# Optimization experiments

Measured on AMD Instinct MI355X. Metric: run time of the kernel, lower is better.

The kernel has to match this reference:

```python
import jax, jax.numpy as jnp
import numpy as np

BATCH = 16384
N_IN = 128
CTX = 128
H = 1024
NB = 8                      # num_bins
OUT_MULT = 3 * NB - 1       # widths + heights + derivatives for RQS
TAIL = 3.0                  # tail_bound
SCALE = float(np.sqrt((H * H) // 2))  # sqrt(prod(hidden_dims)//len(hidden_dims))
MIN_W = 1e-3; MIN_H = 1e-3; MIN_D = 1e-3
DPAD = float(np.log(np.exp(1.0 - MIN_D) - 1.0))  # softplus(DPAD)+MIN_D == 1 at boundaries


def _masks():
    # Standard sequential MADE masks. Input degrees 1..n_in, hidden degrees cycle.
    deg_in = np.arange(1, N_IN + 1)
    deg_h = (np.arange(H) % (N_IN - 1)) + 1
    m0 = deg_h[:, None] >= deg_in[None, :]          # [H, N_IN]
    m1 = deg_h[:, None] >= deg_h[None, :]           # [H, H]
    deg_out = np.repeat(deg_in, OUT_MULT)           # matches view(b, n_in, out_mult)
    m2 = deg_out[:, None] > deg_h[None, :]          # [N_IN*OUT_MULT, H]
    return jnp.asarray(m0), jnp.asarray(m1), jnp.asarray(m2)


def setup_inputs() -> dict:
    key = jax.random.key(0)
    k = jax.random.split(key, 6)
    def rn(kk, shape, fan_in):
        return (jax.random.normal(kk, shape, dtype=jnp.float32) * np.sqrt(1.0 / fan_in)).astype(jnp.float32)
    m0, m1, m2 = _masks()
    return {
        "x": jax.random.normal(k[0], (BATCH, N_IN), dtype=jnp.float32),
        "context": jax.random.normal(k[1], (BATCH, CTX), dtype=jnp.float32),
        "ctx_w": rn(k[2], (H, CTX), CTX),
        "w0": rn(k[3], (H, N_IN), N_IN), "b0": jnp.zeros((H,), jnp.float32),
        "w1": rn(k[4], (H, H), H),       "b1": jnp.zeros((H,), jnp.float32),
        "w2": rn(k[5], (N_IN * OUT_MULT, H), H), "b2": jnp.zeros((N_IN * OUT_MULT,), jnp.float32),
        "mask0": m0, "mask1": m1, "mask2": m2,
    }


def _rqs(x, uw, uh, ud):
    # x: [B, D]; uw, uh: [B, D, NB]; ud: [B, D, NB-1]
    inside = jnp.abs(x) <= TAIL
    xc = jnp.clip(x, -TAIL, TAIL)

    w = MIN_W + (1.0 - MIN_W * NB) * jax.nn.softmax(uw, axis=-1)
    cw = jnp.cumsum(w, axis=-1)
    cw = jnp.concatenate([jnp.zeros_like(cw[..., :1]), cw], axis=-1)
    cw = 2.0 * TAIL * cw - TAIL
    cw = cw.at[..., 0].set(-TAIL).at[..., -1].set(TAIL)
    widths = cw[..., 1:] - cw[..., :-1]

    h = MIN_H + (1.0 - MIN_H * NB) * jax.nn.softmax(uh, axis=-1)
    ch = jnp.cumsum(h, axis=-1)
    ch = jnp.concatenate([jnp.zeros_like(ch[..., :1]), ch], axis=-1)
    ch = 2.0 * TAIL * ch - TAIL
    ch = ch.at[..., 0].set(-TAIL).at[..., -1].set(TAIL)
    heights = ch[..., 1:] - ch[..., :-1]

    pad = jnp.full(ud.shape[:-1] + (1,), DPAD, ud.dtype)
    d = MIN_D + jax.nn.softplus(jnp.concatenate([pad, ud, pad], axis=-1))  # [B, D, NB+1]

    # bucketize: bin index per element (NB is small; comparison-sum beats searchsorted here)
    idx = jnp.clip(jnp.sum((xc[..., None] >= cw).astype(jnp.int32), axis=-1) - 1, 0, NB - 1)
    g = lambda a, i: jnp.take_along_axis(a, i[..., None], axis=-1)[..., 0]

    in_cw = g(cw, idx); in_w = g(widths, idx)
    in_ch = g(ch, idx); in_h = g(heights, idx)
    delta = in_h / in_w
    d0 = g(d, idx); d1 = g(d, idx + 1)

    theta = (xc - in_cw) / in_w
    t1m = theta * (1.0 - theta)
    denom = delta + (d0 + d1 - 2.0 * delta) * t1m
    num = in_h * (delta * theta * theta + d0 * t1m)
    y = in_ch + num / denom
    logdet = (2.0 * jnp.log(delta)
              + jnp.log(d1 * theta * theta + 2.0 * delta * t1m + d0 * (1.0 - theta) ** 2)
              - 2.0 * jnp.log(denom))

    y = jnp.where(inside, y, x)          # identity linear tails
    logdet = jnp.where(inside, logdet, 0.0)
    return y, logdet


def reference(x, context, ctx_w, w0, b0, w1, b1, w2, b2, mask0, mask1, mask2):
    m0 = mask0.astype(w0.dtype); m1 = mask1.astype(w1.dtype); m2 = mask2.astype(w2.dtype)
    hdn = jax.nn.relu(context @ ctx_w.T + x @ (w0 * m0).T + b0)
    hdn = jax.nn.relu(hdn @ (w1 * m1).T + b1)
    out = (hdn @ (w2 * m2).T + b2).reshape(-1, N_IN, OUT_MULT)
    uw = out[..., :NB] / SCALE
    uh = out[..., NB:2 * NB] / SCALE
    ud = out[..., 2 * NB:]
    y, ld = _rqs(x, uw, uh, ud)
    return y, jnp.sum(ld, axis=-1)
```

## Files before the change

### kernel.cpp

```cpp
#include <hip/hip_runtime.h>
#include <cstdint>
#include <cstddef>

#define BATCH   16384
#define N_IN    128
#define CTX     128
#define HDIM    1024
#define NB      8
#define OUT_MULT 23
#define OUT_PAD 24
#define NOUTP   (N_IN * OUT_PAD)
#define KCAT    (CTX + N_IN)

typedef __bf16 bf16x8 __attribute__((ext_vector_type(8)));
typedef float  f32x4  __attribute__((ext_vector_type(4)));

__device__ __forceinline__ uint16_t f2bf(float f) {
    union { float f; uint32_t u; } v; v.f = f;
    uint32_t u = v.u;
    u += 0x7FFFu + ((u >> 16) & 1u);
    return (uint16_t)(u >> 16);
}

__device__ __forceinline__ int kpref_dev(int d) {
    return (d <= 8) ? 9 * d : 72 + 8 * (d - 8);
}
__device__ __forceinline__ int dpos_dev(int p) {
    return (p < 72) ? (p / 9) : (8 + ((p - 72) >> 3));
}
__device__ __forceinline__ int h_of(int p) {
    if (p < 72) { int d = p / 9, j = p - 9 * d; return d + 127 * j; }
    int q = p - 72; int d = 8 + (q >> 3); int j = q & 7; return d + 127 * j;
}

__device__ __forceinline__ void async_ld16(const void* g, const void* l) {
    __builtin_amdgcn_global_load_lds(
        (__attribute__((address_space(1))) void*)(uintptr_t)g,
        (__attribute__((address_space(3))) void*)(uint32_t)(uintptr_t)l,
        16, 0, 0);
}


__global__ void pack_all(
    const float* __restrict__ x,    const float* __restrict__ ctx,
    const float* __restrict__ ctx_w,const float* __restrict__ w0,
    const float* __restrict__ b0,   const float* __restrict__ w1,
    const float* __restrict__ b1,   const float* __restrict__ w2,
    const float* __restrict__ b2,
    uint16_t* __restrict__ xcat, uint16_t* __restrict__ wcat,
    uint16_t* __restrict__ w1m,  uint16_t* __restrict__ w2p,
    float* __restrict__ b0p, float* __restrict__ b1p, float* __restrict__ b2p,
    float* __restrict__ ldz)
{
    __shared__ float srow[HDIM];
    const int blk = blockIdx.x;
    const int tid = threadIdx.x;

    if (blk < 4096) {
        int idx4 = (blk * 256 + tid) * 4;
        int b = idx4 >> 8, c = idx4 & 255;
        f32x4 v = (c < CTX) ? *(const f32x4*)(ctx + (b << 7) + c)
                            : *(const f32x4*)(x   + (b << 7) + (c - CTX));
        ushort4 o;
        o.x = f2bf(v[0]); o.y = f2bf(v[1]); o.z = f2bf(v[2]); o.w = f2bf(v[3]);
        *(ushort4*)(xcat + idx4) = o;
    } else if (blk < 5120) {
        int idx = (blk - 4096) * 256 + tid;
        int p = idx >> 8, c = idx & 255;
        int h = h_of(p);
        float v;
        if (c < CTX) v = ctx_w[(h << 7) + c];
        else {
            int col = c - CTX;
            v = (dpos_dev(p) >= col) ? w0[(h << 7) + col] : 0.0f;
        }
        wcat[idx] = f2bf(v);
    } else if (blk < 6144) {
        const int po = blk - 5120;
        const int drow = dpos_dev(po);
        const float* src = w1 + (size_t)h_of(po) * HDIM;
        *((f32x4*)srow + tid) = *((const f32x4*)src + tid);
        __syncthreads();
        ushort4 o;
#pragma unroll
        for (int e = 0; e < 4; ++e) {
            int pi = 4 * tid + e;
            float v = (drow >= dpos_dev(pi)) ? srow[h_of(pi)] : 0.0f;
            ((uint16_t*)&o)[e] = f2bf(v);
        }
        *((ushort4*)(w1m + (size_t)po * HDIM) + tid) = o;
    } else if (blk < 9216) {
        const int oo = blk - 6144;
        const int g = oo / OUT_PAD, t = oo - g * OUT_PAD;
        const bool live = (t < OUT_MULT);
        if (live) {
            const float* src = w2 + (size_t)(g * OUT_MULT + t) * HDIM;
            *((f32x4*)srow + tid) = *((const f32x4*)src + tid);
        }
        __syncthreads();
        ushort4 o;
#pragma unroll
        for (int e = 0; e < 4; ++e) {
            int pi = 4 * tid + e;
            float v = (live && g > dpos_dev(pi)) ? srow[h_of(pi)] : 0.0f;
            ((uint16_t*)&o)[e] = f2bf(v);
        }
        *((ushort4*)(w2p + (size_t)oo * HDIM) + tid) = o;
    } else if (blk < 9232) {
        int idx = (blk - 9216) * 256 + tid;
        if (idx < HDIM) {
            int h = h_of(idx);
            b0p[idx] = b0[h];
            b1p[idx] = b1[h];
        } else {
            int oo = idx - HDIM;
            int g = oo / OUT_PAD, t = oo - g * OUT_PAD;
            b2p[oo] = (t < OUT_MULT) ? b2[g * OUT_MULT + t] : 0.0f;
        }
    } else {
        int idx = (blk - 9232) * 256 + tid;
        ldz[idx] = 0.0f;
    }
}


template<int MODE>
__device__ __forceinline__ void gemm_bt_body(
    const uint16_t* __restrict__ A,
    const uint16_t* __restrict__ B,
    const float*    __restrict__ bias,
    uint16_t*       __restrict__ C,
    int N, int K, int NT)
{
    __shared__ __align__(16) uint16_t sA[128 * 64];
    __shared__ __align__(16) uint16_t sB[128 * 64];

    const int GM    = 64;
    const int per   = GM * NT;
    const int id    = blockIdx.x;
    const int grp   = id / per;
    const int rem   = id - grp * per;
    const int mt    = grp * GM + (rem & (GM - 1));
    const int nt    = (NT - 1) - (rem >> 6);
    const int bm    = mt << 7;
    const int bn    = nt << 7;

    int K_eff;
    if (MODE == 0)      { int dmax = dpos_dev(bn + 127); K_eff = 128 + dmax + 1; }
    else                { int dmax = dpos_dev(bn + 127); K_eff = kpref_dev(dmax + 1); }
    K_eff = min(K, (K_eff + 63) & ~63);

    const int tid   = threadIdx.x;
    const int wid   = tid >> 6;
    const int lane  = tid & 63;
    const int wm    = (wid & 1) << 6;
    const int wn    = (wid >> 1) << 6;
    const int lrow  = lane & 15;
    const int lquad = lane >> 4;

    const f32x4 vzero = {0.0f, 0.0f, 0.0f, 0.0f};
    f32x4 acc[4][4];
#pragma unroll
    for (int i = 0; i < 4; ++i)
#pragma unroll
        for (int j = 0; j < 4; ++j) acc[i][j] = vzero;

    int goff[4];
#pragma unroll
    for (int t = 0; t < 4; ++t) {
        int c = t * 256 + tid;
        int row = c >> 3, j = c & 7;
        int oct = j ^ (row & 7);
        goff[t] = row * K * 2 + oct * 16;
    }
    const char* gA = (const char*)(A + (size_t)bm * K);
    const char* gB = (const char*)(B + (size_t)bn * K);

    const int octx = lrow & 7;
    const uint16_t* rA = sA + (wm + lrow) * 64;
    const uint16_t* rB = sB + (wn + lrow) * 64;

    for (int k0 = 0; k0 < K_eff; k0 += 64) {
        __syncthreads();
        const int kb = k0 * 2;
#pragma unroll
        for (int t = 0; t < 4; ++t) {
            const int ldsoff = (t * 256 + (wid << 6)) * 16;
            async_ld16(gA + goff[t] + kb, (const char*)sA + ldsoff);
            async_ld16(gB + goff[t] + kb, (const char*)sB + ldsoff);
        }
        __syncthreads();

#pragma unroll
        for (int ks = 0; ks < 2; ++ks) {
            const int oct = ((ks << 2) | lquad) ^ octx;
            bf16x8 af[4], bfr[4];
#pragma unroll
            for (int i = 0; i < 4; ++i) af[i]  = *(const bf16x8*)(rA + i * 1024 + oct * 8);
#pragma unroll
            for (int j = 0; j < 4; ++j) bfr[j] = *(const bf16x8*)(rB + j * 1024 + oct * 8);
#pragma unroll
            for (int i = 0; i < 4; ++i)
#pragma unroll
                for (int j = 0; j < 4; ++j)
                    acc[i][j] = __builtin_amdgcn_mfma_f32_16x16x32_bf16(
                                    af[i], bfr[j], acc[i][j], 0, 0, 0);
        }
    }

#pragma unroll
    for (int j = 0; j < 4; ++j) {
        const int col = bn + wn + j * 16 + lrow;
        const float bv = bias[col];
#pragma unroll
        for (int i = 0; i < 4; ++i) {
            const int row0 = bm + wm + i * 16 + (lquad << 2);
#pragma unroll
            for (int r = 0; r < 4; ++r) {
                float v = fmaxf(acc[i][j][r] + bv, 0.0f);
                C[(size_t)(row0 + r) * N + col] = f2bf(v);
            }
        }
    }
}

__global__ __launch_bounds__(256, 4) void gemm1_k(
    const uint16_t* __restrict__ A, const uint16_t* __restrict__ B,
    const float* __restrict__ bias, uint16_t* __restrict__ C,
    int N, int K, int NT)
{ gemm_bt_body<0>(A, B, bias, C, N, K, NT); }

__global__ __launch_bounds__(256, 4) void gemm2_k(
    const uint16_t* __restrict__ A, const uint16_t* __restrict__ B,
    const float* __restrict__ bias, uint16_t* __restrict__ C,
    int N, int K, int NT)
{ gemm_bt_body<1>(A, B, bias, C, N, K, NT); }


__device__ __forceinline__ float frcp(float v) { return __builtin_amdgcn_rcpf(v); }
__device__ __forceinline__ float softplusf(float v) {
    return fmaxf(v, 0.0f) + __logf(1.0f + __expf(-fabsf(v)));
}

__device__ __forceinline__ void spline_eval(const float* __restrict__ pp,
                                            float xv, float& yout, float& ldout)
{
    float p[OUT_MULT];
#pragma unroll
    for (int k = 0; k < OUT_MULT; ++k) p[k] = pp[k];

    const float TAILF = 3.0f;
    const float MIN_W = 0.001f, MIN_H = 0.001f, MIN_D = 0.001f;
    const float INV_SCALE = 1.0f / 724.0773439350246f;

    const float xc = fminf(fmaxf(xv, -TAILF), TAILF);

    float uw[NB], uh[NB];
#pragma unroll
    for (int k = 0; k < NB; ++k) { uw[k] = p[k] * INV_SCALE; uh[k] = p[NB + k] * INV_SCALE; }
    float mw = uw[0], mh = uh[0];
#pragma unroll
    for (int k = 1; k < NB; ++k) { mw = fmaxf(mw, uw[k]); mh = fmaxf(mh, uh[k]); }
    float ew[NB], eh[NB], sw = 0.0f, sh = 0.0f;
#pragma unroll
    for (int k = 0; k < NB; ++k) {
        ew[k] = __expf(uw[k] - mw); sw += ew[k];
        eh[k] = __expf(uh[k] - mh); sh += eh[k];
    }
    const float FACW = (1.0f - MIN_W * NB) * frcp(sw);
    const float FACH = (1.0f - MIN_H * NB) * frcp(sh);

    float cw[NB + 1], ch[NB + 1];
    cw[0] = -TAILF; ch[0] = -TAILF;
    float aw = 0.0f, ah = 0.0f;
#pragma unroll
    for (int k = 0; k < NB; ++k) {
        aw += MIN_W + FACW * ew[k];
        ah += MIN_H + FACH * eh[k];
        cw[k + 1] = (k == NB - 1) ? TAILF : 2.0f * TAILF * aw - TAILF;
        ch[k + 1] = (k == NB - 1) ? TAILF : 2.0f * TAILF * ah - TAILF;
    }

    float dd[NB + 1];
    dd[0]  = 1.0f;
    dd[NB] = 1.0f;
#pragma unroll
    for (int k = 1; k < NB; ++k) dd[k] = MIN_D + softplusf(p[2 * NB + (k - 1)]);

    float in_cw = cw[0], cw_n = cw[1], in_ch = ch[0], ch_n = ch[1];
    float d0 = dd[0], d1 = dd[1];
#pragma unroll
    for (int k = 1; k < NB; ++k) {
        const bool ge = (xc >= cw[k]);
        in_cw = ge ? cw[k]     : in_cw;
        cw_n  = ge ? cw[k + 1] : cw_n;
        in_ch = ge ? ch[k]     : in_ch;
        ch_n  = ge ? ch[k + 1] : ch_n;
        d0    = ge ? dd[k]     : d0;
        d1    = ge ? dd[k + 1] : d1;
    }
    const float in_w  = cw_n - in_cw;
    const float in_h  = ch_n - in_ch;
    const float inv_w = frcp(in_w);
    const float delta = in_h * inv_w;
    const float theta = (xc - in_cw) * inv_w;
    const float omt   = 1.0f - theta;
    const float t1m   = theta * omt;
    const float denom = delta + (d0 + d1 - 2.0f * delta) * t1m;
    const float num   = in_h * (delta * theta * theta + d0 * t1m);
    float yv = in_ch + num * frcp(denom);
    float ld = 2.0f * __logf(delta)
             + __logf(d1 * theta * theta + 2.0f * delta * t1m + d0 * omt * omt)
             - 2.0f * __logf(denom);
    const bool inside = fabsf(xv) <= TAILF;
    yout  = inside ? yv : xv;
    ldout = inside ? ld : 0.0f;
}


__global__ __launch_bounds__(256, 5) void gemm3_spline(
    const uint16_t* __restrict__ A,
    const uint16_t* __restrict__ B,
    const float*    __restrict__ bias,
    const float*    __restrict__ x,
    float* __restrict__ y,
    float* __restrict__ ldsum)
{
    __shared__ __align__(16) char smem[28672];
    uint16_t* sA = (uint16_t*)smem;
    uint16_t* sB = (uint16_t*)(smem + 16384);
    float* ep    = (float*)smem;

    const int NT  = 32;
    const int per = 64 * NT;
    const int id  = blockIdx.x;
    const int grp = id / per;
    const int rem = id - grp * per;
    const int mt  = grp * 64 + (rem & 63);
    const int nt  = 31 - (rem >> 6);
    const int bm  = mt << 7;
    const int bn  = nt * 96;

    const int K = HDIM;
    int K_eff = kpref_dev(4 * nt + 3);
    K_eff = min(K, (K_eff + 63) & ~63);

    const int tid   = threadIdx.x;
    const int wid   = tid >> 6;
    const int lane  = tid & 63;
    const int wm    = (wid & 1) << 6;
    const int wn    = (wid >> 1) * 48;
    const int lrow  = lane & 15;
    const int lquad = lane >> 4;

    const f32x4 vzero = {0.0f, 0.0f, 0.0f, 0.0f};
    f32x4 acc[4][3];
#pragma unroll
    for (int i = 0; i < 4; ++i)
#pragma unroll
        for (int j = 0; j < 3; ++j) acc[i][j] = vzero;

    int goffA[4], goffB[3];
#pragma unroll
    for (int t = 0; t < 4; ++t) {
        int c = t * 256 + tid;
        int row = c >> 3, j = c & 7;
        goffA[t] = row * K * 2 + (j ^ (row & 7)) * 16;
    }
#pragma unroll
    for (int t = 0; t < 3; ++t) {
        int c = t * 256 + tid;
        int row = c >> 3, j = c & 7;
        goffB[t] = row * K * 2 + (j ^ (row & 7)) * 16;
    }
    const char* gA = (const char*)(A + (size_t)bm * K);
    const char* gB = (const char*)(B + (size_t)bn * K);

    const int octx = lrow & 7;
    const uint16_t* rA = sA + (wm + lrow) * 64;
    const uint16_t* rB = sB + (wn + lrow) * 64;

    for (int k0 = 0; k0 < K_eff; k0 += 64) {
        __syncthreads();
        const int kb = k0 * 2;
#pragma unroll
        for (int t = 0; t < 4; ++t) {
            const int ldsoff = (t * 256 + (wid << 6)) * 16;
            async_ld16(gA + goffA[t] + kb, (const char*)sA + ldsoff);
            if (t < 3)
                async_ld16(gB + goffB[t] + kb, (const char*)sB + ldsoff);
        }
        __syncthreads();

#pragma unroll
        for (int ks = 0; ks < 2; ++ks) {
            const int oct = ((ks << 2) | lquad) ^ octx;
            bf16x8 af[4], bfr[3];
#pragma unroll
            for (int i = 0; i < 4; ++i) af[i]  = *(const bf16x8*)(rA + i * 1024 + oct * 8);
#pragma unroll
            for (int j = 0; j < 3; ++j) bfr[j] = *(const bf16x8*)(rB + j * 1024 + oct * 8);
#pragma unroll
            for (int i = 0; i < 4; ++i)
#pragma unroll
                for (int j = 0; j < 3; ++j)
                    acc[i][j] = __builtin_amdgcn_mfma_f32_16x16x32_bf16(
                                    af[i], bfr[j], acc[i][j], 0, 0, 0);
        }
    }

    __syncthreads();

#pragma unroll
    for (int ph = 0; ph < 2; ++ph) {
        if ((wid & 1) == ph) {
#pragma unroll
            for (int j = 0; j < 3; ++j) {
                const int col = wn + j * 16 + lrow;
                const float bv = bias[bn + col];
#pragma unroll
                for (int i = 0; i < 4; ++i) {
                    const int r0 = i * 16 + (lquad << 2);
#pragma unroll
                    for (int r = 0; r < 4; ++r)
                        ep[(r0 + r) * 100 + col] = acc[i][j][r] + bv;
                }
            }
        }
        __syncthreads();

        {
            const int row  = tid >> 2;
            const int sg   = tid & 3;
            const int grow = bm + (ph << 6) + row;
            const float xv = x[(size_t)grow * N_IN + (4 * nt + sg)];
            float yv, ld;
            spline_eval(ep + row * 100 + sg * OUT_PAD, xv, yv, ld);
            y[(size_t)grow * N_IN + 4 * nt + sg] = yv;

            ld += __shfl_xor(ld, 1, 64);
            ld += __shfl_xor(ld, 2, 64);
            if (sg == 0) atomicAdd(&ldsum[grow], ld);
        }
        if (ph == 0) __syncthreads();
    }
}


extern "C" void kernel_launch(void* const* d_in, const int* in_sizes, int n_in,
                              void* d_out, int out_size, void* d_ws, size_t ws_size,
                              hipStream_t stream)
{
    const float* x     = (const float*)d_in[0];
    const float* ctx   = (const float*)d_in[1];
    const float* ctx_w = (const float*)d_in[2];
    const float* w0    = (const float*)d_in[3];
    const float* b0    = (const float*)d_in[4];
    const float* w1    = (const float*)d_in[5];
    const float* b1    = (const float*)d_in[6];
    const float* w2    = (const float*)d_in[7];
    const float* b2    = (const float*)d_in[8];

    char* ws = (char*)d_ws;
    const size_t XCAT_B = (size_t)BATCH * KCAT * 2;
    const size_t H_B    = (size_t)BATCH * HDIM * 2;
    const size_t WCAT_B = (size_t)HDIM * KCAT * 2;
    const size_t W1_B   = (size_t)HDIM * HDIM * 2;
    const size_t W2P_B  = (size_t)NOUTP * HDIM * 2;

    uint16_t* xcat = (uint16_t*)(ws);
    uint16_t* h1   = (uint16_t*)(ws + XCAT_B);
    uint16_t* h2   = (uint16_t*)(ws + XCAT_B + H_B);
    uint16_t* wcat = (uint16_t*)(ws + XCAT_B + 2 * H_B);
    uint16_t* w1m  = (uint16_t*)(ws + XCAT_B + 2 * H_B + WCAT_B);
    uint16_t* w2p  = (uint16_t*)(ws + XCAT_B + 2 * H_B + WCAT_B + W1_B);
    float*    b0p  = (float*)   (ws + XCAT_B + 2 * H_B + WCAT_B + W1_B + W2P_B);
    float*    b1p  = b0p + HDIM;
    float*    b2p  = b1p + HDIM;

    float* yout  = (float*)d_out;
    float* ldout = yout + (size_t)BATCH * N_IN;

    pack_all<<<9296, 256, 0, stream>>>(x, ctx, ctx_w, w0, b0, w1, b1, w2, b2,
                                       xcat, wcat, w1m, w2p, b0p, b1p, b2p,
                                       ldout);

    const dim3 blk(256);
    gemm1_k<<<dim3(128 * (HDIM / 128)), blk, 0, stream>>>(
        xcat, wcat, b0p, h1, HDIM, KCAT, HDIM / 128);
    gemm2_k<<<dim3(128 * (HDIM / 128)), blk, 0, stream>>>(
        h1, w1m, b1p, h2, HDIM, HDIM, HDIM / 128);
    gemm3_spline<<<dim3(128 * 32), blk, 0, stream>>>(
        h2, w2p, b2p, x, yout, ldout);
}
```

Before: 216.9 us.

## Load GEMM A operand directly into registers, bypassing shared memory

In both GEMM kernels, the A operand fragments are now read straight from global memory into registers in MFMA layout, and its LDS staging buffer is removed. Only B is still staged through shared memory. This cuts LDS traffic and footprint, at the cost of uncoalesced 16-byte global loads per lane with no LDS reuse across waves (the two N-side waves reread the same A rows). It also vectorizes the spline parameter load to float4 over the padded 24 entries and lowers gemm3's launch-bounds occupancy hint from 5 to 4.

```diff
diff --git a/kernel.cpp b/kernel.cpp
--- a/kernel.cpp
+++ b/kernel.cpp
@@ -132,7 +132,6 @@
     uint16_t*       __restrict__ C,
     int N, int K, int NT)
 {
-    __shared__ __align__(16) uint16_t sA[128 * 64];
     __shared__ __align__(16) uint16_t sB[128 * 64];
 
     const int GM    = 64;
@@ -173,11 +172,11 @@
         int oct = j ^ (row & 7);
         goff[t] = row * K * 2 + oct * 16;
     }
-    const char* gA = (const char*)(A + (size_t)bm * K);
     const char* gB = (const char*)(B + (size_t)bn * K);
 
+    const uint16_t* pa = A + (size_t)(bm + wm + lrow) * K + lquad * 8;
+
     const int octx = lrow & 7;
-    const uint16_t* rA = sA + (wm + lrow) * 64;
     const uint16_t* rB = sB + (wn + lrow) * 64;
 
     for (int k0 = 0; k0 < K_eff; k0 += 64) {
@@ -186,17 +185,20 @@
 #pragma unroll
         for (int t = 0; t < 4; ++t) {
             const int ldsoff = (t * 256 + (wid << 6)) * 16;
-            async_ld16(gA + goff[t] + kb, (const char*)sA + ldsoff);
             async_ld16(gB + goff[t] + kb, (const char*)sB + ldsoff);
+        }
+        bf16x8 a0[4], a1[4];
+#pragma unroll
+        for (int i = 0; i < 4; ++i) {
+            a0[i] = *(const bf16x8*)(pa + (size_t)(16 * i) * K + k0);
+            a1[i] = *(const bf16x8*)(pa + (size_t)(16 * i) * K + k0 + 32);
         }
         __syncthreads();
 
 #pragma unroll
         for (int ks = 0; ks < 2; ++ks) {
             const int oct = ((ks << 2) | lquad) ^ octx;
-            bf16x8 af[4], bfr[4];
-#pragma unroll
-            for (int i = 0; i < 4; ++i) af[i]  = *(const bf16x8*)(rA + i * 1024 + oct * 8);
+            bf16x8 bfr[4];
 #pragma unroll
             for (int j = 0; j < 4; ++j) bfr[j] = *(const bf16x8*)(rB + j * 1024 + oct * 8);
 #pragma unroll
@@ -204,7 +206,7 @@
 #pragma unroll
                 for (int j = 0; j < 4; ++j)
                     acc[i][j] = __builtin_amdgcn_mfma_f32_16x16x32_bf16(
-                                    af[i], bfr[j], acc[i][j], 0, 0, 0);
+                                    (ks == 0) ? a0[i] : a1[i], bfr[j], acc[i][j], 0, 0, 0);
         }
     }
 
@@ -245,9 +247,10 @@
 __device__ __forceinline__ void spline_eval(const float* __restrict__ pp,
                                             float xv, float& yout, float& ldout)
 {
-    float p[OUT_MULT];
-#pragma unroll
-    for (int k = 0; k < OUT_MULT; ++k) p[k] = pp[k];
+    float p[OUT_PAD];
+#pragma unroll
+    for (int k = 0; k < OUT_PAD / 4; ++k)
+        *(f32x4*)(p + 4 * k) = *(const f32x4*)(pp + 4 * k);
 
     const float TAILF = 3.0f;
     const float MIN_W = 0.001f, MIN_H = 0.001f, MIN_D = 0.001f;
@@ -318,7 +321,7 @@
 }
 
 
-__global__ __launch_bounds__(256, 5) void gemm3_spline(
+__global__ __launch_bounds__(256, 4) void gemm3_spline(
     const uint16_t* __restrict__ A,
     const uint16_t* __restrict__ B,
     const float*    __restrict__ bias,
@@ -326,9 +329,8 @@
     float* __restrict__ y,
     float* __restrict__ ldsum)
 {
-    __shared__ __align__(16) char smem[28672];
-    uint16_t* sA = (uint16_t*)smem;
-    uint16_t* sB = (uint16_t*)(smem + 16384);
+    __shared__ __align__(16) char smem[25600];
+    uint16_t* sB = (uint16_t*)smem;
     float* ep    = (float*)smem;
 
     const int NT  = 32;
@@ -360,44 +362,40 @@
 #pragma unroll
         for (int j = 0; j < 3; ++j) acc[i][j] = vzero;
 
-    int goffA[4], goffB[3];
-#pragma unroll
-    for (int t = 0; t < 4; ++t) {
-        int c = t * 256 + tid;
-        int row = c >> 3, j = c & 7;
-        goffA[t] = row * K * 2 + (j ^ (row & 7)) * 16;
-    }
+    int goffB[3];
 #pragma unroll
     for (int t = 0; t < 3; ++t) {
         int c = t * 256 + tid;
         int row = c >> 3, j = c & 7;
         goffB[t] = row * K * 2 + (j ^ (row & 7)) * 16;
     }
-    const char* gA = (const char*)(A + (size_t)bm * K);
     const char* gB = (const char*)(B + (size_t)bn * K);
 
+    const uint16_t* pa = A + (size_t)(bm + wm + lrow) * K + lquad * 8;
+
     const int octx = lrow & 7;
-    const uint16_t* rA = sA + (wm + lrow) * 64;
     const uint16_t* rB = sB + (wn + lrow) * 64;
 
     for (int k0 = 0; k0 < K_eff; k0 += 64) {
         __syncthreads();
         const int kb = k0 * 2;
 #pragma unroll
-        for (int t = 0; t < 4; ++t) {
+        for (int t = 0; t < 3; ++t) {
             const int ldsoff = (t * 256 + (wid << 6)) * 16;
-            async_ld16(gA + goffA[t] + kb, (const char*)sA + ldsoff);
-            if (t < 3)
-                async_ld16(gB + goffB[t] + kb, (const char*)sB + ldsoff);
+            async_ld16(gB + goffB[t] + kb, (const char*)sB + ldsoff);
+        }
+        bf16x8 a0[4], a1[4];
+#pragma unroll
+        for (int i = 0; i < 4; ++i) {
+            a0[i] = *(const bf16x8*)(pa + (size_t)(16 * i) * K + k0);
+            a1[i] = *(const bf16x8*)(pa + (size_t)(16 * i) * K + k0 + 32);
         }
         __syncthreads();
 
 #pragma unroll
         for (int ks = 0; ks < 2; ++ks) {
             const int oct = ((ks << 2) | lquad) ^ octx;
-            bf16x8 af[4], bfr[3];
-#pragma unroll
-            for (int i = 0; i < 4; ++i) af[i]  = *(const bf16x8*)(rA + i * 1024 + oct * 8);
+            bf16x8 bfr[3];
 #pragma unroll
             for (int j = 0; j < 3; ++j) bfr[j] = *(const bf16x8*)(rB + j * 1024 + oct * 8);
 #pragma unroll
@@ -405,7 +403,7 @@
 #pragma unroll
                 for (int j = 0; j < 3; ++j)
                     acc[i][j] = __builtin_amdgcn_mfma_f32_16x16x32_bf16(
-                                    af[i], bfr[j], acc[i][j], 0, 0, 0);
+                                    (ks == 0) ? a0[i] : a1[i], bfr[j], acc[i][j], 0, 0, 0);
         }
     }
 
```

New measurement: 328.3 us. 1.51x slower.

## Double-buffer LDS tiles in all three GEMM kernels to overlap loads with MFMA

Applied to the files above, without the earlier changes.

Converts the K loop of the GEMM kernels to a two-stage ping-pong shared-memory pipeline, so the next K tile is prefetched asynchronously while MFMAs run on the current one. This removes one barrier per iteration. LDS per block roughly doubles, so the launch bounds drop to 2 blocks per CU and occupancy falls. The spline parameter load is also vectorised into float4 reads.

```diff
diff --git a/kernel.cpp b/kernel.cpp
--- a/kernel.cpp
+++ b/kernel.cpp
@@ -132,8 +132,8 @@
     uint16_t*       __restrict__ C,
     int N, int K, int NT)
 {
-    __shared__ __align__(16) uint16_t sA[128 * 64];
-    __shared__ __align__(16) uint16_t sB[128 * 64];
+    __shared__ __align__(16) uint16_t sA[2][128 * 64];
+    __shared__ __align__(16) uint16_t sB[2][128 * 64];
 
     const int GM    = 64;
     const int per   = GM * NT;
@@ -177,20 +177,26 @@
     const char* gB = (const char*)(B + (size_t)bn * K);
 
     const int octx = lrow & 7;
-    const uint16_t* rA = sA + (wm + lrow) * 64;
-    const uint16_t* rB = sB + (wn + lrow) * 64;
-
-    for (int k0 = 0; k0 < K_eff; k0 += 64) {
-        __syncthreads();
+
+    auto stage = [&](int b, int k0) {
         const int kb = k0 * 2;
 #pragma unroll
         for (int t = 0; t < 4; ++t) {
             const int ldsoff = (t * 256 + (wid << 6)) * 16;
-            async_ld16(gA + goff[t] + kb, (const char*)sA + ldsoff);
-            async_ld16(gB + goff[t] + kb, (const char*)sB + ldsoff);
-        }
-        __syncthreads();
-
+            async_ld16(gA + goff[t] + kb, (const char*)sA[b] + ldsoff);
+            async_ld16(gB + goff[t] + kb, (const char*)sB[b] + ldsoff);
+        }
+    };
+
+    stage(0, 0);
+    __syncthreads();
+
+    int cur = 0;
+    for (int k0 = 0; k0 < K_eff; k0 += 64) {
+        if (k0 + 64 < K_eff) stage(cur ^ 1, k0 + 64);
+
+        const uint16_t* rA = sA[cur] + (wm + lrow) * 64;
+        const uint16_t* rB = sB[cur] + (wn + lrow) * 64;
 #pragma unroll
         for (int ks = 0; ks < 2; ++ks) {
             const int oct = ((ks << 2) | lquad) ^ octx;
@@ -206,6 +212,9 @@
                     acc[i][j] = __builtin_amdgcn_mfma_f32_16x16x32_bf16(
                                     af[i], bfr[j], acc[i][j], 0, 0, 0);
         }
+
+        __syncthreads();
+        cur ^= 1;
     }
 
 #pragma unroll
@@ -224,13 +233,13 @@
     }
 }
 
-__global__ __launch_bounds__(256, 4) void gemm1_k(
+__global__ __launch_bounds__(256, 2) void gemm1_k(
     const uint16_t* __restrict__ A, const uint16_t* __restrict__ B,
     const float* __restrict__ bias, uint16_t* __restrict__ C,
     int N, int K, int NT)
 { gemm_bt_body<0>(A, B, bias, C, N, K, NT); }
 
-__global__ __launch_bounds__(256, 4) void gemm2_k(
+__global__ __launch_bounds__(256, 2) void gemm2_k(
     const uint16_t* __restrict__ A, const uint16_t* __restrict__ B,
     const float* __restrict__ bias, uint16_t* __restrict__ C,
     int N, int K, int NT)
@@ -245,9 +254,10 @@
 __device__ __forceinline__ void spline_eval(const float* __restrict__ pp,
                                             float xv, float& yout, float& ldout)
 {
-    float p[OUT_MULT];
-#pragma unroll
-    for (int k = 0; k < OUT_MULT; ++k) p[k] = pp[k];
+    float p[OUT_PAD];
+#pragma unroll
+    for (int k = 0; k < OUT_PAD / 4; ++k)
+        *(f32x4*)(p + 4 * k) = *(const f32x4*)(pp + 4 * k);
 
     const float TAILF = 3.0f;
     const float MIN_W = 0.001f, MIN_H = 0.001f, MIN_D = 0.001f;
@@ -318,7 +328,7 @@
 }
 
 
-__global__ __launch_bounds__(256, 5) void gemm3_spline(
+__global__ __launch_bounds__(256, 2) void gemm3_spline(
     const uint16_t* __restrict__ A,
     const uint16_t* __restrict__ B,
     const float*    __restrict__ bias,
@@ -326,10 +336,8 @@
     float* __restrict__ y,
     float* __restrict__ ldsum)
 {
-    __shared__ __align__(16) char smem[28672];
-    uint16_t* sA = (uint16_t*)smem;
-    uint16_t* sB = (uint16_t*)(smem + 16384);
-    float* ep    = (float*)smem;
+    __shared__ __align__(16) char smem[57344];
+    float* ep = (float*)smem;
 
     const int NT  = 32;
     const int per = 64 * NT;
@@ -377,21 +385,31 @@
     const char* gB = (const char*)(B + (size_t)bn * K);
 
     const int octx = lrow & 7;
-    const uint16_t* rA = sA + (wm + lrow) * 64;
-    const uint16_t* rB = sB + (wn + lrow) * 64;
-
-    for (int k0 = 0; k0 < K_eff; k0 += 64) {
-        __syncthreads();
+
+    auto stage = [&](int b, int k0) {
         const int kb = k0 * 2;
+        char* dA = smem + b * 16384;
+        char* dB = smem + 32768 + b * 12288;
 #pragma unroll
         for (int t = 0; t < 4; ++t) {
             const int ldsoff = (t * 256 + (wid << 6)) * 16;
-            async_ld16(gA + goffA[t] + kb, (const char*)sA + ldsoff);
+            async_ld16(gA + goffA[t] + kb, dA + ldsoff);
             if (t < 3)
-                async_ld16(gB + goffB[t] + kb, (const char*)sB + ldsoff);
-        }
-        __syncthreads();
-
+                async_ld16(gB + goffB[t] + kb, dB + ldsoff);
+        }
+    };
+
+    stage(0, 0);
+    __syncthreads();
+
+    int cur = 0;
+    for (int k0 = 0; k0 < K_eff; k0 += 64) {
+        if (k0 + 64 < K_eff) stage(cur ^ 1, k0 + 64);
+
+        const uint16_t* rA = (const uint16_t*)(smem + cur * 16384)
+                             + (wm + lrow) * 64;
+        const uint16_t* rB = (const uint16_t*)(smem + 32768 + cur * 12288)
+                             + (wn + lrow) * 64;
 #pragma unroll
         for (int ks = 0; ks < 2; ++ks) {
             const int oct = ((ks << 2) | lquad) ^ octx;
@@ -407,9 +425,10 @@
                     acc[i][j] = __builtin_amdgcn_mfma_f32_16x16x32_bf16(
                                     af[i], bfr[j], acc[i][j], 0, 0, 0);
         }
-    }
-
-    __syncthreads();
+
+        __syncthreads();
+        cur ^= 1;
+    }
 
 #pragma unroll
     for (int ph = 0; ph < 2; ++ph) {
```

Result: slower. 229.6 us (+5.8%).
